# Performance work log

Measured on AMD Instinct MI355X. Metric: run time of the kernel, lower is better.

The kernel has to match this reference:

```python
import jax, jax.numpy as jnp
import numpy as np

NUM_HEADS = 16
EMBED_DIM = 2048
HEAD_DIM = EMBED_DIM // NUM_HEADS        # 128
LATENT_DIM = HEAD_DIM // 4               # 32
GROUPS = HEAD_DIM // LATENT_DIM          # 4 latent sub-heads per q head
B, T = 1, 2048


def setup_inputs() -> dict:
    key = jax.random.key(0)
    ks = jax.random.split(key, 7)
    s_in = 1.0 / np.sqrt(EMBED_DIM)
    x = jax.random.normal(ks[0], (B, T, EMBED_DIM), dtype=jnp.float32)
    # torch Linear weights: [out_features, in_features]
    Wq = jax.random.normal(ks[1], (EMBED_DIM, EMBED_DIM), dtype=jnp.float32) * s_in
    Wk = jax.random.normal(ks[2], (EMBED_DIM, EMBED_DIM), dtype=jnp.float32) * s_in
    Wv = jax.random.normal(ks[3], (EMBED_DIM, EMBED_DIM), dtype=jnp.float32) * s_in
    Wlk = jax.random.normal(ks[4], (NUM_HEADS * LATENT_DIM, EMBED_DIM), dtype=jnp.float32) * s_in
    Wlv = jax.random.normal(ks[5], (NUM_HEADS * LATENT_DIM, EMBED_DIM), dtype=jnp.float32) * s_in
    Wo = jax.random.normal(ks[6], (EMBED_DIM, EMBED_DIM), dtype=jnp.float32) * s_in
    return {"x": x, "Wq": Wq, "Wk": Wk, "Wv": Wv, "Wlk": Wlk, "Wlv": Wlv, "Wo": Wo}


def reference(x, Wq, Wk, Wv, Wlk, Wlv, Wo):
    Bv, Tv, C = x.shape
    # q: [B,T,H,G,Dl]  (each head's 128-dim q split into 4 latent sub-heads)
    q = (x @ Wq.T).reshape(Bv, Tv, NUM_HEADS, GROUPS, LATENT_DIM)
    # latent k/v: [B,T,H,Dl], shared across the G sub-heads of each q head
    lk = (x @ Wlk.T).reshape(Bv, Tv, NUM_HEADS, LATENT_DIM)
    lv = (x @ Wlv.T).reshape(Bv, Tv, NUM_HEADS, LATENT_DIM)
    # k_proj / v_proj outputs are computed but unused in the original forward.
    scale = 1.0 / np.sqrt(HEAD_DIM).astype(np.float32)
    # scores: [B,H,G,T,T]
    scores = jnp.einsum('bthgd,bshd->bhgts', q, lk) * scale
    probs = jax.nn.softmax(scores, axis=-1)
    out = jnp.einsum('bhgts,bshd->bthgd', probs, lv).reshape(Bv, Tv, C)
    return out @ Wo.T
```

## Files before the change

### kernel.cpp

```cpp
#include <hip/hip_runtime.h>
#include <hip/hip_bf16.h>

typedef __bf16 bf16;
typedef __bf16 bf16x4 __attribute__((ext_vector_type(4)));
typedef __bf16 bf16x8 __attribute__((ext_vector_type(8)));
typedef float  f32x4  __attribute__((ext_vector_type(4)));

#define AS1 __attribute__((address_space(1)))
#define AS3 __attribute__((address_space(3)))

__device__ __forceinline__ void gload_lds16(const bf16* g, bf16* l) {
    __builtin_amdgcn_global_load_lds((const AS1 void*)g, (AS3 void*)l, 16, 0, 0);
}

__device__ __forceinline__ void stage8_f32(const float* s, bf16* l) {
    float4 a = *(const float4*)s;
    float4 b = *(const float4*)(s + 4);
    bf16x8 o;
    o[0] = (bf16)a.x; o[1] = (bf16)a.y; o[2] = (bf16)a.z; o[3] = (bf16)a.w;
    o[4] = (bf16)b.x; o[5] = (bf16)b.y; o[6] = (bf16)b.z; o[7] = (bf16)b.w;
    *(bf16x8*)l = o;
}

template <bool AF32, bool BF32>
__device__ __forceinline__ void gemm_core(
    const void* __restrict__ Av, const void* __restrict__ Bv,
    int m0, int n0, int K, f32x4 (&acc)[4][4],
    int wm, int wn, int r16, int q8)
{
    constexpr int LDA = AF32 ? 40 : 32;
    constexpr int LDB = BF32 ? 40 : 32;
    __shared__ __align__(16) bf16 As[2][128 * LDA];
    __shared__ __align__(16) bf16 Bs[2][128 * LDB];

    const int tid = threadIdx.x;
    const int i0 = tid, i1 = tid + 256;
    const int r0 = i0 >> 2, c0 = (i0 & 3) * 8;
    const int r1 = i1 >> 2, c1 = (i1 & 3) * 8;
    const size_t a0 = (size_t)(m0 + r0) * K + c0, a1 = (size_t)(m0 + r1) * K + c1;
    const size_t b0 = (size_t)(n0 + r0) * K + c0, b1 = (size_t)(n0 + r1) * K + c1;

    auto stage = [&](int buf, int k0) {
        if constexpr (AF32) {
            stage8_f32((const float*)Av + a0 + k0, &As[buf][r0 * LDA + c0]);
            stage8_f32((const float*)Av + a1 + k0, &As[buf][r1 * LDA + c1]);
        } else {
            gload_lds16((const bf16*)Av + a0 + k0, &As[buf][i0 * 8]);
            gload_lds16((const bf16*)Av + a1 + k0, &As[buf][i1 * 8]);
        }
        if constexpr (BF32) {
            stage8_f32((const float*)Bv + b0 + k0, &Bs[buf][r0 * LDB + c0]);
            stage8_f32((const float*)Bv + b1 + k0, &Bs[buf][r1 * LDB + c1]);
        } else {
            gload_lds16((const bf16*)Bv + b0 + k0, &Bs[buf][i0 * 8]);
            gload_lds16((const bf16*)Bv + b1 + k0, &Bs[buf][i1 * 8]);
        }
    };

    stage(0, 0);
    __syncthreads();

    int cur = 0;
    for (int k0 = 0; k0 < K; k0 += 32) {
        if (k0 + 32 < K) stage(cur ^ 1, k0 + 32);

        bf16x8 a[4], b[4];
#pragma unroll
        for (int r = 0; r < 4; ++r)
            a[r] = *(const bf16x8*)&As[cur][(wm + r * 16 + r16) * LDA + q8 * 8];
#pragma unroll
        for (int c = 0; c < 4; ++c)
            b[c] = *(const bf16x8*)&Bs[cur][(wn + c * 16 + r16) * LDB + q8 * 8];
#pragma unroll
        for (int r = 0; r < 4; ++r)
#pragma unroll
            for (int c = 0; c < 4; ++c)
                acc[r][c] = __builtin_amdgcn_mfma_f32_16x16x32_bf16(a[r], b[c], acc[r][c], 0, 0, 0);

        asm volatile("s_waitcnt vmcnt(0) lgkmcnt(0)" ::: "memory");
        __builtin_amdgcn_s_barrier();
        __builtin_amdgcn_sched_barrier(0);
        cur ^= 1;
    }
}

__global__ __launch_bounds__(256) void cvt5(
    const float* __restrict__ s0, const float* __restrict__ s1,
    const float* __restrict__ s2, const float* __restrict__ s3,
    const float* __restrict__ s4,
    bf16* __restrict__ d0, bf16* __restrict__ d1, bf16* __restrict__ d2,
    bf16* __restrict__ d3, bf16* __restrict__ d4)
{
    const float* S[5] = {s0, s1, s2, s3, s4};
    bf16*        D[5] = {d0, d1, d2, d3, d4};
    const int    N[5] = {4194304, 4194304, 1048576, 1048576, 4194304};
    int y = blockIdx.y;
    int base = (blockIdx.x * 256 + threadIdx.x) * 8;
    if (base >= N[y]) return;
    stage8_f32(S[y] + base, D[y] + base);
}

template <bool F32>
__global__ __launch_bounds__(256) void proj_kernel_t(
    const void* __restrict__ x, const void* __restrict__ Wq,
    const void* __restrict__ Wlk, const void* __restrict__ Wlv,
    bf16* __restrict__ Q, bf16* __restrict__ LK, bf16* __restrict__ LVt)
{
    const int bx = blockIdx.x, by = blockIdx.y;
    const int tid = threadIdx.x, lane = tid & 63, wave = tid >> 6;
    const int wm = (wave >> 1) * 64, wn = (wave & 1) * 64;
    const int r16 = lane & 15, q8 = lane >> 4;
    f32x4 acc[4][4] = {};

    const void* Bv; int n0;
    if (bx < 16)      { Bv = Wq;  n0 = bx * 128; }
    else if (bx < 20) { Bv = Wlk; n0 = (bx - 16) * 128; }
    else              { Bv = Wlv; n0 = (bx - 20) * 128; }

    gemm_core<F32, F32>(x, Bv, by * 128, n0, 2048, acc, wm, wn, r16, q8);

    if (bx < 20) {
        bf16* C  = (bx < 16) ? Q : LK;
        int ldc  = (bx < 16) ? 2048 : 512;
#pragma unroll
        for (int r = 0; r < 4; ++r)
#pragma unroll
            for (int c = 0; c < 4; ++c)
#pragma unroll
                for (int i = 0; i < 4; ++i) {
                    int row = by * 128 + wm + r * 16 + q8 * 4 + i;
                    int col = n0 + wn + c * 16 + r16;
                    C[(size_t)row * ldc + col] = (bf16)acc[r][c][i];
                }
    } else {
#pragma unroll
        for (int r = 0; r < 4; ++r)
#pragma unroll
            for (int c = 0; c < 4; ++c) {
                int hd = n0 + wn + c * 16 + r16;
                int tb = by * 128 + wm + r * 16 + q8 * 4;
                bf16x4 pk;
#pragma unroll
                for (int i = 0; i < 4; ++i) pk[i] = (bf16)acc[r][c][i];
                *(bf16x4*)&LVt[(size_t)hd * 2048 + tb] = pk;
            }
    }
}

template <bool BF32>
__global__ __launch_bounds__(256) void out_kernel_t(
    const bf16* __restrict__ A, const void* __restrict__ Wo, float* __restrict__ C)
{
    const int tid = threadIdx.x, lane = tid & 63, wave = tid >> 6;
    const int wm = (wave >> 1) * 64, wn = (wave & 1) * 64;
    const int r16 = lane & 15, q8 = lane >> 4;
    f32x4 acc[4][4] = {};
    gemm_core<false, BF32>(A, Wo, blockIdx.y * 128, blockIdx.x * 128, 2048, acc, wm, wn, r16, q8);
#pragma unroll
    for (int r = 0; r < 4; ++r)
#pragma unroll
        for (int c = 0; c < 4; ++c)
#pragma unroll
            for (int i = 0; i < 4; ++i) {
                int row = blockIdx.y * 128 + wm + r * 16 + q8 * 4 + i;
                int col = blockIdx.x * 128 + wn + c * 16 + r16;
                C[(size_t)row * 2048 + col] = acc[r][c][i];
            }
}

__global__ __launch_bounds__(256) void attn4(
    const bf16* __restrict__ Q, const bf16* __restrict__ LK,
    const bf16* __restrict__ LVt, bf16* __restrict__ O)
{
    __shared__ __align__(16) bf16 Ks[2][64 * 32];
    __shared__ __align__(16) bf16 Vs[2][32 * 64];
    __shared__ __align__(16) bf16 Ps[64 * 72];

    const int tid  = threadIdx.x;
    const int lane = tid & 63;
    const int w    = tid >> 6;
    const int r16  = lane & 15;
    const int q8   = lane >> 4;
    const int hg = blockIdx.y, h = hg >> 2, g = hg & 3;
    const int t0 = blockIdx.x * 128;

    bf16x8 qb[2];
#pragma unroll
    for (int p = 0; p < 2; ++p)
        qb[p] = *(const bf16x8*)(Q + (size_t)(t0 + w * 32 + p * 16 + r16) * 2048
                                 + h * 128 + g * 32 + q8 * 8);

    const int kr = tid >> 2;
    const int kq = (tid & 3) ^ ((tid >> 3) & 3);
    const bf16* kg = LK + (size_t)kr * 512 + h * 32 + kq * 8;
    const int vd = tid >> 3;
    const int vq = (tid & 7) ^ ((tid >> 3) & 7);
    const bf16* vg = LVt + (size_t)(h * 32 + vd) * 2048 + vq * 8;

    const int ksw = (r16 >> 1) & 3;
    const int vsw = r16 & 7;

    f32x4 o_acc[2][2] = {};
    float lsum[2] = {0.f, 0.f};
    const float Cc = 0.08838834764831845f * 1.4426950408889634f;
    const f32x4 z = {0.f, 0.f, 0.f, 0.f};

    gload_lds16(kg, &Ks[0][tid * 8]);
    gload_lds16(vg, &Vs[0][tid * 8]);
    __syncthreads();

    int cur = 0;
    for (int sb = 0; sb < 2048; sb += 64) {
        if (sb + 64 < 2048) {
            gload_lds16(kg + (size_t)(sb + 64) * 512, &Ks[cur ^ 1][tid * 8]);
            gload_lds16(vg + (sb + 64),               &Vs[cur ^ 1][tid * 8]);
        }
        const bf16* ks = Ks[cur];
        const bf16* vs = Vs[cur];

#pragma unroll
        for (int p = 0; p < 2; ++p) {
            f32x4 s[4];
            __builtin_amdgcn_s_setprio(1);
#pragma unroll
            for (int c = 0; c < 4; ++c) {
                bf16x8 kb = *(const bf16x8*)&ks[(c * 16 + r16) * 32 + (q8 ^ ksw) * 8];
                s[c] = __builtin_amdgcn_mfma_f32_16x16x32_bf16(kb, qb[p], z, 0, 0, 0);
            }
            __builtin_amdgcn_s_setprio(0);
#pragma unroll
            for (int c = 0; c < 4; ++c) {
                bf16x4 pk;
#pragma unroll
                for (int i = 0; i < 4; ++i) {
                    float pv = exp2f(s[c][i] * Cc);
                    lsum[p] += pv;
                    pk[i] = (bf16)pv;
                }
                *(bf16x4*)&Ps[(w * 16 + r16) * 72 + c * 16 + q8 * 4] = pk;
            }
            __builtin_amdgcn_s_setprio(1);
#pragma unroll
            for (int kk = 0; kk < 2; ++kk) {
                bf16x8 ap = *(const bf16x8*)&Ps[(w * 16 + r16) * 72 + kk * 32 + q8 * 8];
#pragma unroll
                for (int ct = 0; ct < 2; ++ct) {
                    bf16x8 vb = *(const bf16x8*)&vs[(ct * 16 + r16) * 64
                                                    + (((kk * 4 + q8) ^ vsw) * 8)];
                    o_acc[p][ct] = __builtin_amdgcn_mfma_f32_16x16x32_bf16(ap, vb, o_acc[p][ct], 0, 0, 0);
                }
            }
            __builtin_amdgcn_s_setprio(0);
        }

        asm volatile("s_waitcnt vmcnt(0) lgkmcnt(0)" ::: "memory");
        __builtin_amdgcn_s_barrier();
        __builtin_amdgcn_sched_barrier(0);
        cur ^= 1;
    }

#pragma unroll
    for (int p = 0; p < 2; ++p) {
        float l = lsum[p];
        l += __shfl_xor(l, 16);
        l += __shfl_xor(l, 32);
        float ls[4];
#pragma unroll
        for (int i = 0; i < 4; ++i) ls[i] = __shfl(l, q8 * 4 + i);
#pragma unroll
        for (int ct = 0; ct < 2; ++ct)
#pragma unroll
            for (int i = 0; i < 4; ++i) {
                float o = o_acc[p][ct][i] / ls[i];
                int t = t0 + w * 32 + p * 16 + q8 * 4 + i;
                int d = ct * 16 + r16;
                O[(size_t)t * 2048 + h * 128 + g * 32 + d] = (bf16)o;
            }
    }
}

extern "C" void kernel_launch(void* const* d_in, const int* in_sizes, int n_in,
                              void* d_out, int out_size, void* d_ws, size_t ws_size,
                              hipStream_t stream) {
    const float* x   = (const float*)d_in[0];
    const float* Wq  = (const float*)d_in[1];
    const float* Wlk = (const float*)d_in[4];
    const float* Wlv = (const float*)d_in[5];
    const float* Wo  = (const float*)d_in[6];
    float* out = (float*)d_out;

    const size_t M4 = 4194304, M1 = 1048576;
    const size_t need_fast = (M1 + M1 + M4 + M4 + M1 + M1) * 2;

    if (ws_size >= need_fast) {
        bf16* xb   = (bf16*)d_out;
        bf16* Wqb  = xb + M4;
        bf16* p    = (bf16*)d_ws;
        bf16* Wlkb = p; p += M1;
        bf16* Wlvb = p; p += M1;
        bf16* Wob  = p; p += M4;
        bf16* Qp   = p; p += M4;
        bf16* LKp  = p; p += M1;
        bf16* LVt  = p;
        bf16* ATT  = Qp;

        cvt5<<<dim3(2048, 5), 256, 0, stream>>>(x, Wq, Wlk, Wlv, Wo,
                                                xb, Wqb, Wlkb, Wlvb, Wob);
        proj_kernel_t<false><<<dim3(24, 16), 256, 0, stream>>>(xb, Wqb, Wlkb, Wlvb,
                                                               Qp, LKp, LVt);
        attn4<<<dim3(16, 64), 256, 0, stream>>>(Qp, LKp, LVt, ATT);
        out_kernel_t<false><<<dim3(16, 16), 256, 0, stream>>>(ATT, Wob, out);
    } else {
        bf16* Qp  = (bf16*)d_ws;
        bf16* LKp = Qp + M4;
        bf16* LVt = LKp + M1;
        bf16* ATT = Qp;

        proj_kernel_t<true><<<dim3(24, 16), 256, 0, stream>>>(x, Wq, Wlk, Wlv,
                                                              Qp, LKp, LVt);
        attn4<<<dim3(16, 64), 256, 0, stream>>>(Qp, LKp, LVt, ATT);
        out_kernel_t<true><<<dim3(16, 16), 256, 0, stream>>>(ATT, Wo, out);
    }
}
```

Measured before the change: 309.1 us.

## Double attention query tile per block, hoist K/V fragment loads, fold softmax scale into Q

The attention kernel now handles 256 query rows per block (4 sub-tiles per wave instead of 2), so each K/V tile staged in LDS serves twice as many queries. The K and V MFMA fragments are loaded from LDS once per key block and reused across all sub-tiles instead of being reloaded for each. The softmax scale and log2(e) factor are folded into the Q projection epilogue, removing a multiply per score. In exchange the block count halves (512 blocks), register and LDS use rise (the P buffer grows fourfold), and Q is now rounded to bf16 after scaling.

```diff
diff --git a/kernel.cpp b/kernel.cpp
--- a/kernel.cpp
+++ b/kernel.cpp
@@ -122,6 +122,7 @@
     if (bx < 20) {
         bf16* C  = (bx < 16) ? Q : LK;
         int ldc  = (bx < 16) ? 2048 : 512;
+        const float sc = (bx < 16) ? 0.08838834764831845f * 1.4426950408889634f : 1.0f;
 #pragma unroll
         for (int r = 0; r < 4; ++r)
 #pragma unroll
@@ -130,7 +131,7 @@
                 for (int i = 0; i < 4; ++i) {
                     int row = by * 128 + wm + r * 16 + q8 * 4 + i;
                     int col = n0 + wn + c * 16 + r16;
-                    C[(size_t)row * ldc + col] = (bf16)acc[r][c][i];
+                    C[(size_t)row * ldc + col] = (bf16)(acc[r][c][i] * sc);
                 }
     } else {
 #pragma unroll
@@ -168,13 +169,13 @@
             }
 }
 
-__global__ __launch_bounds__(256) void attn4(
+__global__ __launch_bounds__(256) void attn5(
     const bf16* __restrict__ Q, const bf16* __restrict__ LK,
     const bf16* __restrict__ LVt, bf16* __restrict__ O)
 {
     __shared__ __align__(16) bf16 Ks[2][64 * 32];
     __shared__ __align__(16) bf16 Vs[2][32 * 64];
-    __shared__ __align__(16) bf16 Ps[64 * 72];
+    __shared__ __align__(16) bf16 Ps[256 * 72];
 
     const int tid  = threadIdx.x;
     const int lane = tid & 63;
@@ -182,12 +183,12 @@
     const int r16  = lane & 15;
     const int q8   = lane >> 4;
     const int hg = blockIdx.y, h = hg >> 2, g = hg & 3;
-    const int t0 = blockIdx.x * 128;
-
-    bf16x8 qb[2];
-#pragma unroll
-    for (int p = 0; p < 2; ++p)
-        qb[p] = *(const bf16x8*)(Q + (size_t)(t0 + w * 32 + p * 16 + r16) * 2048
+    const int t0 = blockIdx.x * 256;
+
+    bf16x8 qb[4];
+#pragma unroll
+    for (int p = 0; p < 4; ++p)
+        qb[p] = *(const bf16x8*)(Q + (size_t)(t0 + w * 64 + p * 16 + r16) * 2048
                                  + h * 128 + g * 32 + q8 * 8);
 
     const int kr = tid >> 2;
@@ -200,9 +201,8 @@
     const int ksw = (r16 >> 1) & 3;
     const int vsw = r16 & 7;
 
-    f32x4 o_acc[2][2] = {};
-    float lsum[2] = {0.f, 0.f};
-    const float Cc = 0.08838834764831845f * 1.4426950408889634f;
+    f32x4 o_acc[4][2] = {};
+    float lsum[4] = {0.f, 0.f, 0.f, 0.f};
     const f32x4 z = {0.f, 0.f, 0.f, 0.f};
 
     gload_lds16(kg, &Ks[0][tid * 8]);
@@ -218,37 +218,44 @@
         const bf16* ks = Ks[cur];
         const bf16* vs = Vs[cur];
 
-#pragma unroll
-        for (int p = 0; p < 2; ++p) {
+        bf16x8 kb[4], vb[2][2];
+#pragma unroll
+        for (int c = 0; c < 4; ++c)
+            kb[c] = *(const bf16x8*)&ks[(c * 16 + r16) * 32 + (q8 ^ ksw) * 8];
+#pragma unroll
+        for (int kk = 0; kk < 2; ++kk)
+#pragma unroll
+            for (int ct = 0; ct < 2; ++ct)
+                vb[kk][ct] = *(const bf16x8*)&vs[(ct * 16 + r16) * 64
+                                                 + (((kk * 4 + q8) ^ vsw) * 8)];
+
+#pragma unroll
+        for (int p = 0; p < 4; ++p) {
             f32x4 s[4];
             __builtin_amdgcn_s_setprio(1);
 #pragma unroll
-            for (int c = 0; c < 4; ++c) {
-                bf16x8 kb = *(const bf16x8*)&ks[(c * 16 + r16) * 32 + (q8 ^ ksw) * 8];
-                s[c] = __builtin_amdgcn_mfma_f32_16x16x32_bf16(kb, qb[p], z, 0, 0, 0);
-            }
+            for (int c = 0; c < 4; ++c)
+                s[c] = __builtin_amdgcn_mfma_f32_16x16x32_bf16(kb[c], qb[p], z, 0, 0, 0);
             __builtin_amdgcn_s_setprio(0);
 #pragma unroll
             for (int c = 0; c < 4; ++c) {
                 bf16x4 pk;
 #pragma unroll
                 for (int i = 0; i < 4; ++i) {
-                    float pv = exp2f(s[c][i] * Cc);
+                    float pv = exp2f(s[c][i]);
                     lsum[p] += pv;
                     pk[i] = (bf16)pv;
                 }
-                *(bf16x4*)&Ps[(w * 16 + r16) * 72 + c * 16 + q8 * 4] = pk;
+                *(bf16x4*)&Ps[(size_t)(p * 64 + w * 16 + r16) * 72 + c * 16 + q8 * 4] = pk;
             }
             __builtin_amdgcn_s_setprio(1);
 #pragma unroll
             for (int kk = 0; kk < 2; ++kk) {
-                bf16x8 ap = *(const bf16x8*)&Ps[(w * 16 + r16) * 72 + kk * 32 + q8 * 8];
-#pragma unroll
-                for (int ct = 0; ct < 2; ++ct) {
-                    bf16x8 vb = *(const bf16x8*)&vs[(ct * 16 + r16) * 64
-                                                    + (((kk * 4 + q8) ^ vsw) * 8)];
-                    o_acc[p][ct] = __builtin_amdgcn_mfma_f32_16x16x32_bf16(ap, vb, o_acc[p][ct], 0, 0, 0);
-                }
+                bf16x8 ap = *(const bf16x8*)&Ps[(size_t)(p * 64 + w * 16 + r16) * 72
+                                                + kk * 32 + q8 * 8];
+#pragma unroll
+                for (int ct = 0; ct < 2; ++ct)
+                    o_acc[p][ct] = __builtin_amdgcn_mfma_f32_16x16x32_bf16(ap, vb[kk][ct], o_acc[p][ct], 0, 0, 0);
             }
             __builtin_amdgcn_s_setprio(0);
         }
@@ -260,7 +267,7 @@
     }
 
 #pragma unroll
-    for (int p = 0; p < 2; ++p) {
+    for (int p = 0; p < 4; ++p) {
         float l = lsum[p];
         l += __shfl_xor(l, 16);
         l += __shfl_xor(l, 32);
@@ -272,7 +279,7 @@
 #pragma unroll
             for (int i = 0; i < 4; ++i) {
                 float o = o_acc[p][ct][i] / ls[i];
-                int t = t0 + w * 32 + p * 16 + q8 * 4 + i;
+                int t = t0 + w * 64 + p * 16 + q8 * 4 + i;
                 int d = ct * 16 + r16;
                 O[(size_t)t * 2048 + h * 128 + g * 32 + d] = (bf16)o;
             }
@@ -308,7 +315,7 @@
                                                 xb, Wqb, Wlkb, Wlvb, Wob);
         proj_kernel_t<false><<<dim3(24, 16), 256, 0, stream>>>(xb, Wqb, Wlkb, Wlvb,
                                                                Qp, LKp, LVt);
-        attn4<<<dim3(16, 64), 256, 0, stream>>>(Qp, LKp, LVt, ATT);
+        attn5<<<dim3(8, 64), 256, 0, stream>>>(Qp, LKp, LVt, ATT);
         out_kernel_t<false><<<dim3(16, 16), 256, 0, stream>>>(ATT, Wob, out);
     } else {
         bf16* Qp  = (bf16*)d_ws;
@@ -318,7 +325,7 @@
 
         proj_kernel_t<true><<<dim3(24, 16), 256, 0, stream>>>(x, Wq, Wlk, Wlv,
                                                               Qp, LKp, LVt);
-        attn4<<<dim3(16, 64), 256, 0, stream>>>(Qp, LKp, LVt, ATT);
+        attn5<<<dim3(8, 64), 256, 0, stream>>>(Qp, LKp, LVt, ATT);
         out_kernel_t<true><<<dim3(16, 16), 256, 0, stream>>>(ATT, Wo, out);
     }
 }
```

After: 312.2 us. No clear change (+1.0%).
